# Optimization experiments

Measured on AMD Instinct MI355X. Metric: run time of the kernel, lower is better.

## Reference

```python
import jax, jax.numpy as jnp
import numpy as np

B_SZ, L, N, H = 8, 4096, 256, 256
R_MIN, R_MAX, MAX_PHASE = 0.0, 1.0, 0.314


def setup_inputs() -> dict:
    key = jax.random.key(0)
    ks = jax.random.split(key, 8)
    x = jax.random.normal(ks[0], (B_SZ, L, H), jnp.float32)
    def glorot(k, shape):
        return jax.random.normal(k, shape, jnp.float32) * jnp.sqrt(2.0 / (shape[0] + shape[1])).astype(jnp.float32)
    B_re = glorot(ks[1], (N, H))
    B_im = glorot(ks[2], (N, H))
    C_re = glorot(ks[3], (H, N))
    C_im = glorot(ks[4], (H, N))
    # DiskRingRadius / DiskRingPhase initializers
    u1 = jax.random.uniform(ks[5], (N,), jnp.float32, 1e-6, 1.0)
    u2 = jax.random.uniform(ks[6], (N,), jnp.float32, 1e-6, 1.0)
    nu_log = jnp.log(-0.5 * jnp.log(u1 * (R_MAX ** 2 - R_MIN ** 2) + R_MIN ** 2))
    theta_log = jnp.log(MAX_PHASE * u2)
    D = jax.random.normal(ks[7], (H,), jnp.float32) * 0.05  # RandomNormal(stddev=0.05)
    return dict(x=x, B_re=B_re, B_im=B_im, C_re=C_re, C_im=C_im,
                nu_log=nu_log, theta_log=theta_log, D=D)


def reference(x, B_re, B_im, C_re, C_im, nu_log, theta_log, D):
    # Diagonal complex recurrence parameters
    Lambda = jnp.exp(jax.lax.complex(-jnp.exp(nu_log), jnp.exp(theta_log)))  # [N]
    gamma = jnp.sqrt(1.0 - jnp.abs(Lambda) ** 2).astype(jnp.complex64)       # [N]
    B_norm = (B_re + 1j * B_im).astype(jnp.complex64) * gamma[:, None]       # [N,H]
    C = (C_re + 1j * C_im).astype(jnp.complex64)                             # [H,N]

    # Input projection: [B,L,N] complex
    Bu = jnp.einsum('blh,nh->bln', x.astype(jnp.complex64), B_norm)
    Lambda_el = jnp.broadcast_to(Lambda, Bu.shape)

    def combine(a, b):
        la, ba = a
        lb, bb = b
        return (la * lb, lb * ba + bb)

    _, states = jax.lax.associative_scan(combine, (Lambda_el, Bu), axis=1)  # [B,L,N]

    y = jnp.real(jnp.einsum('bln,hn->blh', states, C))
    y = y + x * D  # H_in == H -> elementwise skip
    return y
```

## Files before the change

kernel.cpp:

```cpp
#include <hip/hip_runtime.h>
#include <hip/hip_bf16.h>
#include <math.h>

#define B_SZ 8
#define LSEQ 4096
#define NDIM 256
#define HDIM 256
#define MROWS (B_SZ * LSEQ)
#define CH 64
#define NC (LSEQ / CH)

#define BM 64
#define BN 128
#define BK 32
#define PAD 40

typedef _Float16 half8 __attribute__((ext_vector_type(8)));
typedef float fx4 __attribute__((ext_vector_type(4)));

__global__ void k_prep(const float* __restrict__ Bre, const float* __restrict__ Bim,
                       const float* __restrict__ Cre, const float* __restrict__ Cim,
                       const float* __restrict__ nu_log, const float* __restrict__ th_log,
                       _Float16* __restrict__ BreH, _Float16* __restrict__ BimH,
                       _Float16* __restrict__ CreH, _Float16* __restrict__ CimNH,
                       float* __restrict__ lamRe, float* __restrict__ lamIm) {
    int r = blockIdx.x;
    int t = threadIdx.x;
    float nu  = expf(nu_log[r]);
    float th  = expf(th_log[r]);
    float mod = expf(-nu);
    float g   = sqrtf(fmaxf(1.0f - mod * mod, 0.0f));
    if (t == 0) {
        lamRe[r] = mod * cosf(th);
        lamIm[r] = mod * sinf(th);
    }
    int i = r * 256 + t;
    BreH[i]  = (_Float16)(Bre[i] * g);
    BimH[i]  = (_Float16)(Bim[i] * g);
    CreH[i]  = (_Float16)Cre[i];
    CimNH[i] = (_Float16)(-Cim[i]);
}

__global__ void k_pow(const float* __restrict__ nu_log, const float* __restrict__ th_log,
                      float* __restrict__ powRe, float* __restrict__ powIm) {
    int i = blockIdx.x;
    int n = threadIdx.x;
    float nu = expf(nu_log[n]);
    float th = expf(th_log[n]);
    float k  = (float)(i + 1);
    float mod = expf(-nu * k);
    powRe[i * 256 + n] = mod * cosf(th * k);
    powIm[i * 256 + n] = mod * sinf(th * k);
}

__launch_bounds__(256)
__global__ void k_bu(const float* __restrict__ x,
                     const _Float16* __restrict__ BreH,
                     const _Float16* __restrict__ BimH,
                     _Float16* __restrict__ buReH,
                     _Float16* __restrict__ buImH) {
    __shared__ __align__(16) _Float16 As[2][BM * PAD];
    __shared__ __align__(16) _Float16 Br[2][BN * PAD];
    __shared__ __align__(16) _Float16 Bi[2][BN * PAD];

    const int tid  = threadIdx.x;
    const int lane = tid & 63;
    const int wave = tid >> 6;
    const int wr   = wave >> 1;
    const int wc   = wave & 1;
    const int m0   = blockIdx.x * BM;
    const int n0   = blockIdx.y * BN;

    const int ar = tid >> 2, ac = (tid & 3) * 8;
    const int br = tid >> 1, bc = (tid & 1) * 16;

    const int fRC = lane & 15;
    const int fKg = (lane >> 4) * 8;

    fx4 accR[8], accI[8];
#pragma unroll
    for (int i = 0; i < 8; ++i) { accR[i] = (fx4)0.0f; accI[i] = (fx4)0.0f; }

    float4 xf0, xf1;
    half8 wr0, wr1, wi0, wi1;

    {
        const float* xp = x + (size_t)(m0 + ar) * HDIM + ac;
        xf0 = *(const float4*)xp;
        xf1 = *(const float4*)(xp + 4);
        const _Float16* bp1 = BreH + (size_t)(n0 + br) * HDIM + bc;
        const _Float16* bp2 = BimH + (size_t)(n0 + br) * HDIM + bc;
        wr0 = *(const half8*)bp1;       wr1 = *(const half8*)(bp1 + 8);
        wi0 = *(const half8*)bp2;       wi1 = *(const half8*)(bp2 + 8);
        half8 hv;
        hv[0]=(_Float16)xf0.x; hv[1]=(_Float16)xf0.y; hv[2]=(_Float16)xf0.z; hv[3]=(_Float16)xf0.w;
        hv[4]=(_Float16)xf1.x; hv[5]=(_Float16)xf1.y; hv[6]=(_Float16)xf1.z; hv[7]=(_Float16)xf1.w;
        *(half8*)&As[0][ar * PAD + ac] = hv;
        *(half8*)&Br[0][br * PAD + bc] = wr0;  *(half8*)&Br[0][br * PAD + bc + 8] = wr1;
        *(half8*)&Bi[0][br * PAD + bc] = wi0;  *(half8*)&Bi[0][br * PAD + bc + 8] = wi1;
    }
    __syncthreads();

    int p = 0;
    for (int k0 = 0; k0 < HDIM; k0 += BK) {
        const bool nx = (k0 + BK) < HDIM;
        if (nx) {
            const float* xp = x + (size_t)(m0 + ar) * HDIM + k0 + BK + ac;
            xf0 = *(const float4*)xp;
            xf1 = *(const float4*)(xp + 4);
            const _Float16* bp1 = BreH + (size_t)(n0 + br) * HDIM + k0 + BK + bc;
            const _Float16* bp2 = BimH + (size_t)(n0 + br) * HDIM + k0 + BK + bc;
            wr0 = *(const half8*)bp1;   wr1 = *(const half8*)(bp1 + 8);
            wi0 = *(const half8*)bp2;   wi1 = *(const half8*)(bp2 + 8);
        }
        half8 af[2], bRf[4], bIf[4];
#pragma unroll
        for (int sm = 0; sm < 2; ++sm)
            af[sm] = *(const half8*)&As[p][(wr * 32 + sm * 16 + fRC) * PAD + fKg];
#pragma unroll
        for (int sn = 0; sn < 4; ++sn) {
            bRf[sn] = *(const half8*)&Br[p][(wc * 64 + sn * 16 + fRC) * PAD + fKg];
            bIf[sn] = *(const half8*)&Bi[p][(wc * 64 + sn * 16 + fRC) * PAD + fKg];
        }
#pragma unroll
        for (int sm = 0; sm < 2; ++sm)
#pragma unroll
            for (int sn = 0; sn < 4; ++sn) {
                accR[sm * 4 + sn] = __builtin_amdgcn_mfma_f32_16x16x32_f16(af[sm], bRf[sn], accR[sm * 4 + sn], 0, 0, 0);
                accI[sm * 4 + sn] = __builtin_amdgcn_mfma_f32_16x16x32_f16(af[sm], bIf[sn], accI[sm * 4 + sn], 0, 0, 0);
            }
        if (nx) {
            int pn = p ^ 1;
            half8 hv;
            hv[0]=(_Float16)xf0.x; hv[1]=(_Float16)xf0.y; hv[2]=(_Float16)xf0.z; hv[3]=(_Float16)xf0.w;
            hv[4]=(_Float16)xf1.x; hv[5]=(_Float16)xf1.y; hv[6]=(_Float16)xf1.z; hv[7]=(_Float16)xf1.w;
            *(half8*)&As[pn][ar * PAD + ac] = hv;
            *(half8*)&Br[pn][br * PAD + bc] = wr0;  *(half8*)&Br[pn][br * PAD + bc + 8] = wr1;
            *(half8*)&Bi[pn][br * PAD + bc] = wi0;  *(half8*)&Bi[pn][br * PAD + bc + 8] = wi1;
        }
        __syncthreads();
        p ^= 1;
    }

    const int rBase = (lane >> 4) * 4;
#pragma unroll
    for (int sm = 0; sm < 2; ++sm)
#pragma unroll
        for (int sn = 0; sn < 4; ++sn) {
            int n = n0 + wc * 64 + sn * 16 + fRC;
#pragma unroll
            for (int reg = 0; reg < 4; ++reg) {
                int m = m0 + wr * 32 + sm * 16 + rBase + reg;
                size_t idx = (size_t)m * NDIM + n;
                buReH[idx] = (_Float16)accR[sm * 4 + sn][reg];
                buImH[idx] = (_Float16)accI[sm * 4 + sn][reg];
            }
        }
}

__launch_bounds__(256)
__global__ void k_scan1(_Float16* __restrict__ buReH,
                        _Float16* __restrict__ buImH,
                        const float* __restrict__ lamRe,
                        const float* __restrict__ lamIm,
                        float* __restrict__ finRe,
                        float* __restrict__ finIm) {
    const int c = blockIdx.x;
    const int b = blockIdx.y;
    const int n = threadIdx.x;
    const float lr = lamRe[n];
    const float li = lamIm[n];
    size_t base = ((size_t)b * LSEQ + (size_t)c * CH) * NDIM + n;
    float sr = 0.0f, si = 0.0f;
#pragma unroll 8
    for (int i = 0; i < CH; ++i) {
        size_t idx = base + (size_t)i * NDIM;
        float ur = (float)buReH[idx];
        float ui = (float)buImH[idx];
        float nr = fmaf(lr, sr, fmaf(-li, si, ur));
        float ni = fmaf(lr, si, fmaf(li, sr, ui));
        sr = nr; si = ni;
        buReH[idx] = (_Float16)sr;
        buImH[idx] = (_Float16)si;
    }
    size_t fidx = ((size_t)b * NC + c) * NDIM + n;
    finRe[fidx] = sr;
    finIm[fidx] = si;
}

__launch_bounds__(256)
__global__ void k_carry(const float* __restrict__ lamRe,
                        const float* __restrict__ lamIm,
                        const float* __restrict__ finRe,
                        const float* __restrict__ finIm,
                        float* __restrict__ carRe,
                        float* __restrict__ carIm) {
    const int b = blockIdx.x;
    const int n = threadIdx.x;
    const float lr = lamRe[n];
    const float li = lamIm[n];
    float kr = 1.0f, ki = 0.0f;
#pragma unroll
    for (int i = 0; i < CH; ++i) {
        float t = kr * lr - ki * li;
        ki = fmaf(kr, li, ki * lr);
        kr = t;
    }
    float cr = 0.0f, ci = 0.0f;
    for (int c = 0; c < NC; ++c) {
        size_t idx = ((size_t)b * NC + c) * NDIM + n;
        carRe[idx] = cr;
        carIm[idx] = ci;
        float fr = finRe[idx];
        float fi = finIm[idx];
        float t = fmaf(kr, cr, fmaf(-ki, ci, fr));
        ci = fmaf(kr, ci, fmaf(ki, cr, fi));
        cr = t;
    }
}

__launch_bounds__(256)
__global__ void k_out(const _Float16* __restrict__ sReH,
                      const _Float16* __restrict__ sImH,
                      const _Float16* __restrict__ CreH,
                      const _Float16* __restrict__ CimNH,
                      const float* __restrict__ powRe,
                      const float* __restrict__ powIm,
                      const float* __restrict__ carRe,
                      const float* __restrict__ carIm,
                      const float* __restrict__ x,
                      const float* __restrict__ Dv,
                      float* __restrict__ y) {
    __shared__ __align__(16) _Float16 A1[2][BM * PAD];
    __shared__ __align__(16) _Float16 A2[2][BM * PAD];
    __shared__ __align__(16) _Float16 Cr[2][BN * PAD];
    __shared__ __align__(16) _Float16 Ci[2][BN * PAD];

    const int tid  = threadIdx.x;
    const int lane = tid & 63;
    const int wave = tid >> 6;
    const int wr   = wave >> 1;
    const int wc   = wave & 1;
    const int m0   = blockIdx.x * BM;
    const int h0   = blockIdx.y * BN;
    const int chunk = m0 >> 6;

    const int ar = tid >> 2, ac = (tid & 3) * 8;
    const int br = tid >> 1, bc = (tid & 1) * 16;

    const int fRC = lane & 15;
    const int fKg = (lane >> 4) * 8;

    fx4 acc[8];
#pragma unroll
    for (int i = 0; i < 8; ++i) acc[i] = (fx4)0.0f;

    half8 s1, s2, c0a, c0b, c1a, c1b;
    float4 pr0, pr1, pi0, pi1, cr0, cr1, ci0, ci1;

#define LOAD_STAGE(K0)                                                          \
    {                                                                           \
        size_t aOff = (size_t)(m0 + ar) * NDIM + (K0) + ac;                     \
        s1 = *(const half8*)(sReH + aOff);                                      \
        s2 = *(const half8*)(sImH + aOff);                                      \
        size_t pOff = (size_t)ar * NDIM + (K0) + ac;                            \
        pr0 = *(const float4*)(powRe + pOff); pr1 = *(const float4*)(powRe + pOff + 4); \
        pi0 = *(const float4*)(powIm + pOff); pi1 = *(const float4*)(powIm + pOff + 4); \
        size_t cOff = (size_t)chunk * NDIM + (K0) + ac;                         \
        cr0 = *(const float4*)(carRe + cOff); cr1 = *(const float4*)(carRe + cOff + 4); \
        ci0 = *(const float4*)(carIm + cOff); ci1 = *(const float4*)(carIm + cOff + 4); \
        const _Float16* cp1 = CreH  + (size_t)(h0 + br) * NDIM + (K0) + bc;     \
        const _Float16* cp2 = CimNH + (size_t)(h0 + br) * NDIM + (K0) + bc;     \
        c0a = *(const half8*)cp1;  c0b = *(const half8*)(cp1 + 8);              \
        c1a = *(const half8*)cp2;  c1b = *(const half8*)(cp2 + 8);              \
    }

#define WRITE_STAGE(P)                                                          \
    {                                                                           \
        float prA[8] = {pr0.x,pr0.y,pr0.z,pr0.w,pr1.x,pr1.y,pr1.z,pr1.w};       \
        float piA[8] = {pi0.x,pi0.y,pi0.z,pi0.w,pi1.x,pi1.y,pi1.z,pi1.w};       \
        float crA[8] = {cr0.x,cr0.y,cr0.z,cr0.w,cr1.x,cr1.y,cr1.z,cr1.w};       \
        float ciA[8] = {ci0.x,ci0.y,ci0.z,ci0.w,ci1.x,ci1.y,ci1.z,ci1.w};       \
        half8 h1, h2;                                                           \
        _Pragma("unroll")                                                       \
        for (int e = 0; e < 8; ++e) {                                           \
            float ur = fmaf(prA[e], crA[e], fmaf(-piA[e], ciA[e], (float)s1[e])); \
            float ui = fmaf(prA[e], ciA[e], fmaf( piA[e], crA[e], (float)s2[e])); \
            h1[e] = (_Float16)ur; h2[e] = (_Float16)ui;                         \
        }                                                                       \
        *(half8*)&A1[P][ar * PAD + ac] = h1;                                    \
        *(half8*)&A2[P][ar * PAD + ac] = h2;                                    \
        *(half8*)&Cr[P][br * PAD + bc] = c0a;  *(half8*)&Cr[P][br * PAD + bc + 8] = c0b; \
        *(half8*)&Ci[P][br * PAD + bc] = c1a;  *(half8*)&Ci[P][br * PAD + bc + 8] = c1b; \
    }

    LOAD_STAGE(0);
    WRITE_STAGE(0);
    __syncthreads();

    int p = 0;
    for (int k0 = 0; k0 < NDIM; k0 += BK) {
        const bool nx = (k0 + BK) < NDIM;
        if (nx) LOAD_STAGE(k0 + BK);
        half8 a1[2], a2[2], bRf[4], bIf[4];
#pragma unroll
        for (int sm = 0; sm < 2; ++sm) {
            a1[sm] = *(const half8*)&A1[p][(wr * 32 + sm * 16 + fRC) * PAD + fKg];
            a2[sm] = *(const half8*)&A2[p][(wr * 32 + sm * 16 + fRC) * PAD + fKg];
        }
#pragma unroll
        for (int sn = 0; sn < 4; ++sn) {
            bRf[sn] = *(const half8*)&Cr[p][(wc * 64 + sn * 16 + fRC) * PAD + fKg];
            bIf[sn] = *(const half8*)&Ci[p][(wc * 64 + sn * 16 + fRC) * PAD + fKg];
        }
#pragma unroll
        for (int sm = 0; sm < 2; ++sm)
#pragma unroll
            for (int sn = 0; sn < 4; ++sn) {
                acc[sm * 4 + sn] = __builtin_amdgcn_mfma_f32_16x16x32_f16(a1[sm], bRf[sn], acc[sm * 4 + sn], 0, 0, 0);
                acc[sm * 4 + sn] = __builtin_amdgcn_mfma_f32_16x16x32_f16(a2[sm], bIf[sn], acc[sm * 4 + sn], 0, 0, 0);
            }
        if (nx) WRITE_STAGE(p ^ 1);
        __syncthreads();
        p ^= 1;
    }

    float d[4];
#pragma unroll
    for (int sn = 0; sn < 4; ++sn) d[sn] = Dv[h0 + wc * 64 + sn * 16 + fRC];

    const int rBase = (lane >> 4) * 4;
#pragma unroll
    for (int sm = 0; sm < 2; ++sm)
#pragma unroll
        for (int sn = 0; sn < 4; ++sn) {
            int h = h0 + wc * 64 + sn * 16 + fRC;
#pragma unroll
            for (int reg = 0; reg < 4; ++reg) {
                int m = m0 + wr * 32 + sm * 16 + rBase + reg;
                size_t idx = (size_t)m * HDIM + h;
                y[idx] = fmaf(x[idx], d[sn], acc[sm * 4 + sn][reg]);
            }
        }
#undef LOAD_STAGE
#undef WRITE_STAGE
}

extern "C" void kernel_launch(void* const* d_in, const int* in_sizes, int n_in,
                              void* d_out, int out_size, void* d_ws, size_t ws_size,
                              hipStream_t stream) {
    const float* x      = (const float*)d_in[0];
    const float* B_re   = (const float*)d_in[1];
    const float* B_im   = (const float*)d_in[2];
    const float* C_re   = (const float*)d_in[3];
    const float* C_im   = (const float*)d_in[4];
    const float* nu_log = (const float*)d_in[5];
    const float* th_log = (const float*)d_in[6];
    const float* D      = (const float*)d_in[7];
    float* y = (float*)d_out;

    char* p = (char*)d_ws;
    _Float16* buReH = (_Float16*)p;  p += (size_t)MROWS * NDIM * 2;
    _Float16* buImH = (_Float16*)p;  p += (size_t)MROWS * NDIM * 2;
    _Float16* BreH  = (_Float16*)p;  p += (size_t)NDIM * HDIM * 2;
    _Float16* BimH  = (_Float16*)p;  p += (size_t)NDIM * HDIM * 2;
    _Float16* CreH  = (_Float16*)p;  p += (size_t)HDIM * NDIM * 2;
    _Float16* CimNH = (_Float16*)p;  p += (size_t)HDIM * NDIM * 2;
    float* lamRe = (float*)p;  p += NDIM * 4;
    float* lamIm = (float*)p;  p += NDIM * 4;
    float* powRe = (float*)p;  p += (size_t)CH * NDIM * 4;
    float* powIm = (float*)p;  p += (size_t)CH * NDIM * 4;
    float* finRe = (float*)p;  p += (size_t)B_SZ * NC * NDIM * 4;
    float* finIm = (float*)p;  p += (size_t)B_SZ * NC * NDIM * 4;
    float* carRe = (float*)p;  p += (size_t)B_SZ * NC * NDIM * 4;
    float* carIm = (float*)p;  p += (size_t)B_SZ * NC * NDIM * 4;

    k_prep<<<NDIM, 256, 0, stream>>>(B_re, B_im, C_re, C_im, nu_log, th_log,
                                     BreH, BimH, CreH, CimNH, lamRe, lamIm);
    k_pow<<<CH, 256, 0, stream>>>(nu_log, th_log, powRe, powIm);

    dim3 gGemm(MROWS / BM, NDIM / BN);
    k_bu<<<gGemm, 256, 0, stream>>>(x, BreH, BimH, buReH, buImH);

    dim3 gScan(NC, B_SZ);
    k_scan1<<<gScan, 256, 0, stream>>>(buReH, buImH, lamRe, lamIm, finRe, finIm);

    k_carry<<<B_SZ, 256, 0, stream>>>(lamRe, lamIm, finRe, finIm, carRe, carIm);

    dim3 gOut(MROWS / BM, HDIM / BN);
    k_out<<<gOut, 256, 0, stream>>>(buReH, buImH, CreH, CimNH,
                                    powRe, powIm, carRe, carIm, x, D, y);
}
```

Measured before the change: 171.8 us.

## Fuse intra-chunk scan into input-projection GEMM epilogue and merge pow into prep

The input-projection GEMM now stages its 64x128 output tile in shared memory (transposed, padded), runs the 64-step chunk-local complex recurrence per column there, then writes scanned states and chunk finals to global. This drops the separate scan kernel and its full read-modify-write pass over the two fp16 state buffers. The lambda-power table is also computed inside the prep kernel, which saves one launch. The cost is that only 128 of 256 threads do the serial scan in the epilogue, and the final global store gathers strided fp16 values from LDS.

```diff
diff --git a/kernel.cpp b/kernel.cpp
--- a/kernel.cpp
+++ b/kernel.cpp
@@ -14,8 +14,10 @@
 #define BN 128
 #define BK 32
 #define PAD 40
+#define SSTR 68
 
 typedef _Float16 half8 __attribute__((ext_vector_type(8)));
+typedef _Float16 half4 __attribute__((ext_vector_type(4)));
 typedef float fx4 __attribute__((ext_vector_type(4)));
 
 __global__ void k_prep(const float* __restrict__ Bre, const float* __restrict__ Bim,
@@ -23,7 +25,8 @@
                        const float* __restrict__ nu_log, const float* __restrict__ th_log,
                        _Float16* __restrict__ BreH, _Float16* __restrict__ BimH,
                        _Float16* __restrict__ CreH, _Float16* __restrict__ CimNH,
-                       float* __restrict__ lamRe, float* __restrict__ lamIm) {
+                       float* __restrict__ lamRe, float* __restrict__ lamIm,
+                       float* __restrict__ powRe, float* __restrict__ powIm) {
     int r = blockIdx.x;
     int t = threadIdx.x;
     float nu  = expf(nu_log[r]);
@@ -39,29 +42,27 @@
     BimH[i]  = (_Float16)(Bim[i] * g);
     CreH[i]  = (_Float16)Cre[i];
     CimNH[i] = (_Float16)(-Cim[i]);
+    if (r < CH) {
+        float nuN = expf(nu_log[t]);
+        float thN = expf(th_log[t]);
+        float k   = (float)(r + 1);
+        float mo  = expf(-nuN * k);
+        powRe[r * 256 + t] = mo * cosf(thN * k);
+        powIm[r * 256 + t] = mo * sinf(thN * k);
+    }
 }
 
-__global__ void k_pow(const float* __restrict__ nu_log, const float* __restrict__ th_log,
-                      float* __restrict__ powRe, float* __restrict__ powIm) {
-    int i = blockIdx.x;
-    int n = threadIdx.x;
-    float nu = expf(nu_log[n]);
-    float th = expf(th_log[n]);
-    float k  = (float)(i + 1);
-    float mod = expf(-nu * k);
-    powRe[i * 256 + n] = mod * cosf(th * k);
-    powIm[i * 256 + n] = mod * sinf(th * k);
-}
-
 __launch_bounds__(256)
-__global__ void k_bu(const float* __restrict__ x,
-                     const _Float16* __restrict__ BreH,
-                     const _Float16* __restrict__ BimH,
-                     _Float16* __restrict__ buReH,
-                     _Float16* __restrict__ buImH) {
-    __shared__ __align__(16) _Float16 As[2][BM * PAD];
-    __shared__ __align__(16) _Float16 Br[2][BN * PAD];
-    __shared__ __align__(16) _Float16 Bi[2][BN * PAD];
+__global__ void k_buscan(const float* __restrict__ x,
+                         const _Float16* __restrict__ BreH,
+                         const _Float16* __restrict__ BimH,
+                         const float* __restrict__ lamRe,
+                         const float* __restrict__ lamIm,
+                         _Float16* __restrict__ stReH,
+                         _Float16* __restrict__ stImH,
+                         float* __restrict__ finRe,
+                         float* __restrict__ finIm) {
+    __shared__ __align__(16) _Float16 smem[25600];
 
     const int tid  = threadIdx.x;
     const int lane = tid & 63;
@@ -82,7 +83,7 @@
     for (int i = 0; i < 8; ++i) { accR[i] = (fx4)0.0f; accI[i] = (fx4)0.0f; }
 
     float4 xf0, xf1;
-    half8 wr0, wr1, wi0, wi1;
+    half8 w0, w1, w2, w3;
 
     {
         const float* xp = x + (size_t)(m0 + ar) * HDIM + ac;
@@ -90,19 +91,20 @@
         xf1 = *(const float4*)(xp + 4);
         const _Float16* bp1 = BreH + (size_t)(n0 + br) * HDIM + bc;
         const _Float16* bp2 = BimH + (size_t)(n0 + br) * HDIM + bc;
-        wr0 = *(const half8*)bp1;       wr1 = *(const half8*)(bp1 + 8);
-        wi0 = *(const half8*)bp2;       wi1 = *(const half8*)(bp2 + 8);
+        w0 = *(const half8*)bp1;  w1 = *(const half8*)(bp1 + 8);
+        w2 = *(const half8*)bp2;  w3 = *(const half8*)(bp2 + 8);
         half8 hv;
         hv[0]=(_Float16)xf0.x; hv[1]=(_Float16)xf0.y; hv[2]=(_Float16)xf0.z; hv[3]=(_Float16)xf0.w;
         hv[4]=(_Float16)xf1.x; hv[5]=(_Float16)xf1.y; hv[6]=(_Float16)xf1.z; hv[7]=(_Float16)xf1.w;
-        *(half8*)&As[0][ar * PAD + ac] = hv;
-        *(half8*)&Br[0][br * PAD + bc] = wr0;  *(half8*)&Br[0][br * PAD + bc + 8] = wr1;
-        *(half8*)&Bi[0][br * PAD + bc] = wi0;  *(half8*)&Bi[0][br * PAD + bc + 8] = wi1;
+        *(half8*)&smem[ar * PAD + ac] = hv;
+        *(half8*)&smem[2560 + br * PAD + bc] = w0;  *(half8*)&smem[2560 + br * PAD + bc + 8] = w1;
+        *(half8*)&smem[7680 + br * PAD + bc] = w2;  *(half8*)&smem[7680 + br * PAD + bc + 8] = w3;
     }
     __syncthreads();
 
     int p = 0;
     for (int k0 = 0; k0 < HDIM; k0 += BK) {
+        const int po = p * 12800;
         const bool nx = (k0 + BK) < HDIM;
         if (nx) {
             const float* xp = x + (size_t)(m0 + ar) * HDIM + k0 + BK + ac;
@@ -110,17 +112,17 @@
             xf1 = *(const float4*)(xp + 4);
             const _Float16* bp1 = BreH + (size_t)(n0 + br) * HDIM + k0 + BK + bc;
             const _Float16* bp2 = BimH + (size_t)(n0 + br) * HDIM + k0 + BK + bc;
-            wr0 = *(const half8*)bp1;   wr1 = *(const half8*)(bp1 + 8);
-            wi0 = *(const half8*)bp2;   wi1 = *(const half8*)(bp2 + 8);
+            w0 = *(const half8*)bp1;  w1 = *(const half8*)(bp1 + 8);
+            w2 = *(const half8*)bp2;  w3 = *(const half8*)(bp2 + 8);
         }
         half8 af[2], bRf[4], bIf[4];
 #pragma unroll
         for (int sm = 0; sm < 2; ++sm)
-            af[sm] = *(const half8*)&As[p][(wr * 32 + sm * 16 + fRC) * PAD + fKg];
+            af[sm] = *(const half8*)&smem[po + (wr * 32 + sm * 16 + fRC) * PAD + fKg];
 #pragma unroll
         for (int sn = 0; sn < 4; ++sn) {
-            bRf[sn] = *(const half8*)&Br[p][(wc * 64 + sn * 16 + fRC) * PAD + fKg];
-            bIf[sn] = *(const half8*)&Bi[p][(wc * 64 + sn * 16 + fRC) * PAD + fKg];
+            bRf[sn] = *(const half8*)&smem[po + 2560 + (wc * 64 + sn * 16 + fRC) * PAD + fKg];
+            bIf[sn] = *(const half8*)&smem[po + 7680 + (wc * 64 + sn * 16 + fRC) * PAD + fKg];
         }
 #pragma unroll
         for (int sm = 0; sm < 2; ++sm)
@@ -130,62 +132,80 @@
                 accI[sm * 4 + sn] = __builtin_amdgcn_mfma_f32_16x16x32_f16(af[sm], bIf[sn], accI[sm * 4 + sn], 0, 0, 0);
             }
         if (nx) {
-            int pn = p ^ 1;
+            const int qo = (p ^ 1) * 12800;
             half8 hv;
             hv[0]=(_Float16)xf0.x; hv[1]=(_Float16)xf0.y; hv[2]=(_Float16)xf0.z; hv[3]=(_Float16)xf0.w;
             hv[4]=(_Float16)xf1.x; hv[5]=(_Float16)xf1.y; hv[6]=(_Float16)xf1.z; hv[7]=(_Float16)xf1.w;
-            *(half8*)&As[pn][ar * PAD + ac] = hv;
-            *(half8*)&Br[pn][br * PAD + bc] = wr0;  *(half8*)&Br[pn][br * PAD + bc + 8] = wr1;
-            *(half8*)&Bi[pn][br * PAD + bc] = wi0;  *(half8*)&Bi[pn][br * PAD + bc + 8] = wi1;
+            *(half8*)&smem[qo + ar * PAD + ac] = hv;
+            *(half8*)&smem[qo + 2560 + br * PAD + bc] = w0;  *(half8*)&smem[qo + 2560 + br * PAD + bc + 8] = w1;
+            *(half8*)&smem[qo + 7680 + br * PAD + bc] = w2;  *(half8*)&smem[qo + 7680 + br * PAD + bc + 8] = w3;
         }
         __syncthreads();
         p ^= 1;
     }
 
+    _Float16* SRe = smem;
+    _Float16* SIm = smem + 8704;
+
     const int rBase = (lane >> 4) * 4;
 #pragma unroll
     for (int sm = 0; sm < 2; ++sm)
 #pragma unroll
         for (int sn = 0; sn < 4; ++sn) {
-            int n = n0 + wc * 64 + sn * 16 + fRC;
+            int col = wc * 64 + sn * 16 + fRC;
+            int row = wr * 32 + sm * 16 + rBase;
+            half4 h1, h2;
 #pragma unroll
             for (int reg = 0; reg < 4; ++reg) {
-                int m = m0 + wr * 32 + sm * 16 + rBase + reg;
-                size_t idx = (size_t)m * NDIM + n;
-                buReH[idx] = (_Float16)accR[sm * 4 + sn][reg];
-                buImH[idx] = (_Float16)accI[sm * 4 + sn][reg];
+                h1[reg] = (_Float16)accR[sm * 4 + sn][reg];
+                h2[reg] = (_Float16)accI[sm * 4 + sn][reg];
             }
-        }
-}
-
-__launch_bounds__(256)
-__global__ void k_scan1(_Float16* __restrict__ buReH,
-                        _Float16* __restrict__ buImH,
-                        const float* __restrict__ lamRe,
-                        const float* __restrict__ lamIm,
-                        float* __restrict__ finRe,
-                        float* __restrict__ finIm) {
-    const int c = blockIdx.x;
-    const int b = blockIdx.y;
-    const int n = threadIdx.x;
-    const float lr = lamRe[n];
-    const float li = lamIm[n];
-    size_t base = ((size_t)b * LSEQ + (size_t)c * CH) * NDIM + n;
-    float sr = 0.0f, si = 0.0f;
+            *(half4*)&SRe[col * SSTR + row] = h1;
+            *(half4*)&SIm[col * SSTR + row] = h2;
+        }
+    __syncthreads();
+
+    if (tid < BN) {
+        int col = tid;
+        int n = n0 + col;
+        float lr = lamRe[n], li = lamIm[n];
+        _Float16* cR = &SRe[col * SSTR];
+        _Float16* cI = &SIm[col * SSTR];
+        float sr = 0.0f, si = 0.0f;
 #pragma unroll 8
-    for (int i = 0; i < CH; ++i) {
-        size_t idx = base + (size_t)i * NDIM;
-        float ur = (float)buReH[idx];
-        float ui = (float)buImH[idx];
-        float nr = fmaf(lr, sr, fmaf(-li, si, ur));
-        float ni = fmaf(lr, si, fmaf(li, sr, ui));
-        sr = nr; si = ni;
-        buReH[idx] = (_Float16)sr;
-        buImH[idx] = (_Float16)si;
-    }
-    size_t fidx = ((size_t)b * NC + c) * NDIM + n;
-    finRe[fidx] = sr;
-    finIm[fidx] = si;
+        for (int r = 0; r < CH; ++r) {
+            float ur = (float)cR[r];
+            float ui = (float)cI[r];
+            float nr = fmaf(lr, sr, fmaf(-li, si, ur));
+            float ni = fmaf(lr, si, fmaf(li, sr, ui));
+            sr = nr; si = ni;
+            cR[r] = (_Float16)sr;
+            cI[r] = (_Float16)si;
+        }
+        int bb = blockIdx.x >> 6, cc = blockIdx.x & 63;
+        size_t f = ((size_t)(bb * NC + cc)) * NDIM + n;
+        finRe[f] = sr;
+        finIm[f] = si;
+    }
+    __syncthreads();
+
+    {
+        int row = tid >> 2;
+        int cb  = (tid & 3) * 32;
+        size_t gbase = (size_t)(m0 + row) * NDIM + n0 + cb;
+#pragma unroll
+        for (int g = 0; g < 4; ++g) {
+            half8 h1, h2;
+#pragma unroll
+            for (int e = 0; e < 8; ++e) {
+                int col = cb + g * 8 + e;
+                h1[e] = SRe[col * SSTR + row];
+                h2[e] = SIm[col * SSTR + row];
+            }
+            *(half8*)(stReH + gbase + g * 8) = h1;
+            *(half8*)(stImH + gbase + g * 8) = h2;
+        }
+    }
 }
 
 __launch_bounds__(256)
@@ -207,6 +227,7 @@
         kr = t;
     }
     float cr = 0.0f, ci = 0.0f;
+#pragma unroll 8
     for (int c = 0; c < NC; ++c) {
         size_t idx = ((size_t)b * NC + c) * NDIM + n;
         carRe[idx] = cr;
@@ -360,8 +381,8 @@
     float* y = (float*)d_out;
 
     char* p = (char*)d_ws;
-    _Float16* buReH = (_Float16*)p;  p += (size_t)MROWS * NDIM * 2;
-    _Float16* buImH = (_Float16*)p;  p += (size_t)MROWS * NDIM * 2;
+    _Float16* stReH = (_Float16*)p;  p += (size_t)MROWS * NDIM * 2;
+    _Float16* stImH = (_Float16*)p;  p += (size_t)MROWS * NDIM * 2;
     _Float16* BreH  = (_Float16*)p;  p += (size_t)NDIM * HDIM * 2;
     _Float16* BimH  = (_Float16*)p;  p += (size_t)NDIM * HDIM * 2;
     _Float16* CreH  = (_Float16*)p;  p += (size_t)HDIM * NDIM * 2;
@@ -376,18 +397,16 @@
     float* carIm = (float*)p;  p += (size_t)B_SZ * NC * NDIM * 4;
 
     k_prep<<<NDIM, 256, 0, stream>>>(B_re, B_im, C_re, C_im, nu_log, th_log,
-                                     BreH, BimH, CreH, CimNH, lamRe, lamIm);
-    k_pow<<<CH, 256, 0, stream>>>(nu_log, th_log, powRe, powIm);
+                                     BreH, BimH, CreH, CimNH, lamRe, lamIm,
+                                     powRe, powIm);
 
     dim3 gGemm(MROWS / BM, NDIM / BN);
-    k_bu<<<gGemm, 256, 0, stream>>>(x, BreH, BimH, buReH, buImH);
-
-    dim3 gScan(NC, B_SZ);
-    k_scan1<<<gScan, 256, 0, stream>>>(buReH, buImH, lamRe, lamIm, finRe, finIm);
+    k_buscan<<<gGemm, 256, 0, stream>>>(x, BreH, BimH, lamRe, lamIm,
+                                        stReH, stImH, finRe, finIm);
 
     k_carry<<<B_SZ, 256, 0, stream>>>(lamRe, lamIm, finRe, finIm, carRe, carIm);
 
     dim3 gOut(MROWS / BM, HDIM / BN);
-    k_out<<<gOut, 256, 0, stream>>>(buReH, buImH, CreH, CimNH,
+    k_out<<<gOut, 256, 0, stream>>>(stReH, stImH, CreH, CimNH,
                                     powRe, powIm, carRe, carIm, x, D, y);
 }
```

Result: faster. 161.8 us (-5.8%).
